# Kernel tuning notes

Hardware: AMD Instinct MI355X
Metric: run time of the kernel (lower is better)

The kernel has to match this reference:

```python
import jax, jax.numpy as jnp
import numpy as np

DIM = 1      # homological dimension
CARD = 50    # number of diagram points
H, W = 28, 28
D = 2        # len(Ip.shape)


def _cubical(X, dim=DIM, card=CARD):
    """Pure-numpy cubical persistence (gudhi semantics: lower-dim cells get the
    min of incident top-dimensional cells; finite pairs of dimension `dim`,
    positive persistence, sorted by persistence descending; returns flat
    (i,j) pixel indices of birth/death critical top cells, zero-padded to
    2*D*card int32 values). Mirrors the Cubical numpy_function in the repo."""
    X = np.asarray(X, dtype=np.float64)
    Hh, Ww = X.shape
    A, Bc = 2 * Hh - 1, 2 * Ww - 1
    n = A * Bc
    F = np.empty(n)                 # filtration value per cell
    P = np.empty(n, np.int64)       # flat pixel index of the top cell realizing F
    dms = np.empty(n, np.int64)     # cell dimension

    def cands(a, lim):
        if a % 2 == 1:
            return [(a - 1) // 2]
        return [r for r in (a // 2 - 1, a // 2) if 0 <= r < lim]

    for a in range(A):
        ris = cands(a, Hh)
        for b in range(Bc):
            cjs = cands(b, Ww)
            best = None
            bp = 0
            for r in ris:
                for c in cjs:
                    v = X[r, c]
                    if best is None or v < best:
                        best = v
                        bp = r * Ww + c
            idx = a * Bc + b
            F[idx] = best
            P[idx] = bp
            dms[idx] = (a & 1) + (b & 1)

    order = np.lexsort((np.arange(n), dms, F))   # sort by (F, dim, index)
    pos = np.empty(n, np.int64)
    pos[order] = np.arange(n)

    def faces(cell):
        a, b = divmod(cell, Bc)
        fs = []
        if a & 1:
            fs += [(a - 1) * Bc + b, (a + 1) * Bc + b]
        if b & 1:
            fs += [a * Bc + b - 1, a * Bc + b + 1]
        return fs

    # standard Z/2 boundary-matrix reduction
    Rcols = {}
    low_to_col = {}
    pairs = []
    for j in range(n):
        cell = order[j]
        col = set(int(pos[f]) for f in faces(cell))
        while col:
            l = max(col)
            k = low_to_col.get(l)
            if k is None:
                break
            col ^= Rcols[k]
        if col:
            l = max(col)
            low_to_col[l] = j
            Rcols[j] = col
            pairs.append((l, j))

    rows, pers = [], []
    for (i, j) in pairs:
        bc, dc = order[i], order[j]
        if dms[bc] != dim:
            continue
        pr = F[dc] - F[bc]
        if pr <= 0:
            continue
        rows.append((int(P[bc]), int(P[dc])))
        pers.append(pr)
    if rows:
        srt = np.argsort(np.asarray(pers))[::-1]   # persistence descending
        rows = [rows[k] for k in srt]

    inds = []
    for k in range(min(card, len(rows))):
        bi, di = rows[k]
        inds += [bi // Ww, bi % Ww, di // Ww, di % Ww]
    inds += [0] * (2 * D * card - len(inds))
    return np.asarray(inds, dtype=np.int32)


def setup_inputs() -> dict:
    key = jax.random.key(0)
    k1, k2 = jax.random.split(key)
    I = jax.random.normal(k1, (H, W, 2), dtype=jnp.float32)
    p = jax.random.normal(k2, (2, 1), dtype=jnp.float32)
    return {"I": I, "p": p}


def reference(I, p):
    # Ip = reshape(tensordot(I, p, 1), [28, 28])
    Ip = jnp.reshape(jnp.tensordot(I, p, 1), (H, W))
    inds = jax.pure_callback(
        lambda x: _cubical(np.asarray(x)),
        jax.ShapeDtypeStruct((2 * D * CARD,), jnp.int32),
        Ip,
    )
    inds = jax.lax.stop_gradient(inds).reshape(-1, D)   # [2*card, 2]
    # gather_nd(Ip, inds) then reshape to [card, 2]
    dgm = Ip[inds[:, 0], inds[:, 1]].reshape(-1, 2)
    return dgm
```

## Files before the change

kernel.cpp:

```cpp
#include <hip/hip_runtime.h>

#define IMG_H 28
#define IMG_W 28
#define AA 55
#define NCELL 3025
#define NEDGE 1512
#define NSQ 729
#define CARD 50
#define NW 24
#define CAP 160
#define BS 1024

typedef unsigned long long u64;
typedef unsigned int u32;
typedef unsigned short u16;

#define OFF_KEYSE   0
#define OFF_KEYSS   16384
#define OFF_IP      24576
#define OFF_RANKE   27712
#define OFF_RANKSQ  30736
#define OFF_COL     0
#define OFF_OWNB    30720
#define OFF_CANDA   0
#define OFF_CANDB   8192
#define OFF_BND     43008
#define OFF_EDGEF   48840
#define OFF_SQF     54888
#define OFF_CURLOW  58448
#define OFF_PAIRLOW 60832
#define OFF_NONAPP  62296
#define OFF_SCAL    63768
#define SMEM_TOTAL  63784

__device__ __forceinline__ int edgeCid(int a, int b) {
    return (a & 1) ? (((a - 1) >> 1) * 28 + (b >> 1))
                   : (756 + (a >> 1) * 27 + ((b - 1) >> 1));
}

__device__ __forceinline__ u32 sortable(float f) {
    u32 fb = __float_as_uint(f);
    return (fb & 0x80000000u) ? ~fb : (fb | 0x80000000u);
}
__device__ __forceinline__ float unsortable(u32 v) {
    return __uint_as_float((v & 0x80000000u) ? (v & 0x7FFFFFFFu) : ~v);
}

__device__ __forceinline__ u64 ldrelax(u64* p) {
    return __hip_atomic_load(p, __ATOMIC_RELAXED, __HIP_MEMORY_SCOPE_WORKGROUP);
}
__device__ __forceinline__ void strelax(u64* p, u64 v) {
    __hip_atomic_store(p, v, __ATOMIC_RELAXED, __HIP_MEMORY_SCOPE_WORKGROUP);
}

__device__ __forceinline__ u64 shflx64(u64 v, int s) {
    u32 lo = __shfl_xor((u32)v, s, 64);
    u32 hi = __shfl_xor((u32)(v >> 32), s, 64);
    return ((u64)hi << 32) | lo;
}

__device__ __forceinline__ void cswapDir(u64& a, u64& b, bool up) {
    u64 mn = a < b ? a : b, mx = a < b ? b : a;
    a = up ? mn : mx; b = up ? mx : mn;
}

__device__ __forceinline__ u64 bstage(u64 v, int i, int s, int size) {
    u64 p = shflx64(v, s);
    bool keepmin = (((i & size) == 0) == ((i & s) == 0));
    return keepmin ? (v < p ? v : p) : (v > p ? v : p);
}

__device__ __forceinline__ void sessA(u64& r0, u64& r1, int i0) {
    for (int size = 2; size <= 64; size <<= 1)
        for (int s = size >> 1; s; s >>= 1) {
            r0 = bstage(r0, i0, s, size);
            r1 = bstage(r1, i0 + 64, s, size);
        }
}
__device__ __forceinline__ void sessB(u64& r0, u64& r1, int i0, int size) {
    bool asc = ((i0 & size) == 0);
    { u64 mn = r0 < r1 ? r0 : r1, mx = r0 < r1 ? r1 : r0;
      r0 = asc ? mn : mx; r1 = asc ? mx : mn; }
    for (int s = 32; s; s >>= 1) {
        bool keep = (asc == ((i0 & s) == 0));
        u64 p0 = shflx64(r0, s);
        r0 = keep ? (r0 < p0 ? r0 : p0) : (r0 > p0 ? r0 : p0);
        u64 p1 = shflx64(r1, s);
        r1 = keep ? (r1 < p1 ? r1 : p1) : (r1 > p1 ? r1 : p1);
    }
}

template<int G>
__device__ __forceinline__ void fusedClassicArr(u64* arr, int nElem) {
    const int nG = nElem / G;
    for (int gid = (int)threadIdx.x; gid < nG; gid += BS) {
        int high = gid >> 7, low = gid & 127;
        bool up = ((high & 1) == 0);
        int base = high * G * 128 + low;
        u64 k[G];
        #pragma unroll
        for (int g = 0; g < G; ++g) k[g] = arr[base + g * 128];
        #pragma unroll
        for (int d = G / 2; d >= 1; d >>= 1)
            #pragma unroll
            for (int g = 0; g < G; ++g)
                if (!(g & d)) cswapDir(k[g], k[g | d], up);
        #pragma unroll
        for (int g = 0; g < G; ++g) arr[base + g * 128] = k[g];
    }
}

__device__ __forceinline__ void sessWin(u64* kE, u64* kS, int i0, int size, bool hasS) {
    u64 a = kE[i0], b = kE[i0 + 64];
    sessB(a, b, i0, size);
    kE[i0] = a; kE[i0 + 64] = b;
    if (hasS) {
        u64 c = kS[i0], d = kS[i0 + 64];
        sessB(c, d, i0, size);
        kS[i0] = c; kS[i0 + 64] = d;
    }
}

__device__ __forceinline__ u64 lstage(u64 v, int lane, int s, bool up) {
    u64 p = shflx64(v, s);
    bool keepmin = (up == ((lane & s) == 0));
    return keepmin ? (v < p ? v : p) : (v > p ? v : p);
}

__device__ __forceinline__ u64 sort64(u64 v, int lane) {
    for (int size = 2; size <= 32; size <<= 1)
        for (int s = size >> 1; s; s >>= 1)
            v = lstage(v, lane, s, (lane & size) == 0);
    for (int s = 32; s; s >>= 1)
        v = lstage(v, lane, s, true);
    return v;
}
__device__ __forceinline__ u64 merge64(u64 a, u64 b, int lane) {
    u64 br = shflx64(b, 63);
    u64 m = a < br ? a : br;
    for (int s = 32; s; s >>= 1)
        m = lstage(m, lane, s, true);
    return m;
}

__device__ __forceinline__ void xorInline(u64 o, u64& w, int lane) {
    #pragma unroll
    for (int q = 0; q < 4; ++q) {
        int rr = (int)((o >> (12 * q)) & 0xFFFull);
        if ((rr >> 6) == lane) w ^= 1ull << (rr & 63);
    }
}

__device__ __forceinline__ int findLow(u64 w, int lane) {
    u64 mask = __ballot(w != 0ull);
    if (mask == 0ull) return 0xFFFE;
    int L = 63 - __builtin_clzll(mask);
    int cand = (lane << 6) + 63 - __builtin_clzll(w | 1ull);
    return __builtin_amdgcn_readlane(cand, L);
}

__device__ __forceinline__ u64 bcast64lane0(u64 v) {
    u32 lo = __builtin_amdgcn_readfirstlane((u32)v);
    u32 hi = __builtin_amdgcn_readfirstlane((u32)(v >> 32));
    return ((u64)hi << 32) | lo;
}

__global__ __launch_bounds__(BS) void cubical_kernel(const float* __restrict__ I,
                                                     const float* __restrict__ p,
                                                     float* __restrict__ out) {
    __shared__ __align__(16) char smem[SMEM_TOTAL];
    u64*    keysE   = (u64*)(smem + OFF_KEYSE);
    u64*    keysS   = (u64*)(smem + OFF_KEYSS);
    float*  Ip      = (float*)(smem + OFF_IP);
    u16*    rankE   = (u16*)(smem + OFF_RANKE);
    u16*    rankSq  = (u16*)(smem + OFF_RANKSQ);
    u64*    col     = (u64*)(smem + OFF_COL);
    u64*    ownerBnd= (u64*)(smem + OFF_OWNB);
    u64*    candA   = (u64*)(smem + OFF_CANDA);
    u64*    candB   = (u64*)(smem + OFF_CANDB);
    u64*    bnd     = (u64*)(smem + OFF_BND);
    float*  edgeFr  = (float*)(smem + OFF_EDGEF);
    float*  sqF     = (float*)(smem + OFF_SQF);
    u16*    curLow  = (u16*)(smem + OFF_CURLOW);
    u16*    pairLow = (u16*)(smem + OFF_PAIRLOW);
    u16*    nonapp  = (u16*)(smem + OFF_NONAPP);
    float*  padvP   = (float*)(smem + OFF_SCAL);
    int*    Mp      = (int*)(smem + OFF_SCAL + 4);
    int*    tickP   = (int*)(smem + OFF_SCAL + 8);

    const int tid = threadIdx.x;
    const int wave = tid >> 6, lane = tid & 63;

    const float p0 = p[0], p1 = p[1];
    for (int i = tid; i < IMG_H * IMG_W; i += BS) {
        float v = I[2 * i] * p0 + I[2 * i + 1] * p1;
        Ip[i] = v;
        if (i == 0) *padvP = v;
    }
    for (int i = 1512 + tid; i < 2048; i += BS) keysE[i] = ~0ull;
    for (int i = 729 + tid; i < 1024; i += BS) keysS[i] = ~0ull;
    __syncthreads();

    for (int idx = tid; idx < NCELL; idx += BS) {
        int a = idx / AA, b = idx % AA;
        int da = a & 1, db = b & 1;
        int dim = da + db;
        if (dim == 0) continue;
        int r0, r1, c0, c1;
        if (da) { r0 = r1 = (a - 1) >> 1; }
        else    { r1 = a >> 1; r0 = (a == 0) ? r1 : r1 - 1; }
        if (db) { c0 = c1 = (b - 1) >> 1; }
        else    { c1 = b >> 1; c0 = (b == 0) ? c1 : c1 - 1; }
        float best = Ip[r0 * IMG_W + c0];
        best = fminf(best, Ip[r0 * IMG_W + c1]);
        best = fminf(best, Ip[r1 * IMG_W + c0]);
        best = fminf(best, Ip[r1 * IMG_W + c1]);
        u64 key = ((u64)sortable(best) << 12) | (u32)idx;
        if (dim == 1) keysE[edgeCid(a, b)] = key;
        else          keysS[((a - 1) >> 1) * 27 + ((b - 1) >> 1)] = key;
    }
    __syncthreads();

    {
        const int eB = wave * 128 + lane;
        const bool hasS = (wave < 8);
        {
            u64 a = keysE[eB], b = keysE[eB + 64];
            sessA(a, b, eB);
            sessB(a, b, eB, 128);
            keysE[eB] = a; keysE[eB + 64] = b;
            if (hasS) {
                u64 c = keysS[eB], d = keysS[eB + 64];
                sessA(c, d, eB);
                sessB(c, d, eB, 128);
                keysS[eB] = c; keysS[eB + 64] = d;
            }
        }
        __syncthreads();
        fusedClassicArr<2>(keysE, 2048);
        fusedClassicArr<2>(keysS, 1024);
        __syncthreads();
        sessWin(keysE, keysS, eB, 256, hasS);
        __syncthreads();
        fusedClassicArr<4>(keysE, 2048);
        fusedClassicArr<4>(keysS, 1024);
        __syncthreads();
        sessWin(keysE, keysS, eB, 512, hasS);
        __syncthreads();
        fusedClassicArr<8>(keysE, 2048);
        fusedClassicArr<8>(keysS, 1024);
        __syncthreads();
        sessWin(keysE, keysS, eB, 1024, hasS);
        __syncthreads();
        fusedClassicArr<16>(keysE, 2048);
        __syncthreads();
        sessWin(keysE, keysS, eB, 2048, false);
        __syncthreads();
    }

    for (int r = tid; r < NEDGE; r += BS) {
        u64 k = keysE[r];
        int idx = (int)(k & 0xFFFull);
        int a = idx / AA, b = idx % AA;
        rankE[edgeCid(a, b)] = (u16)r;
        edgeFr[r] = unsortable((u32)(k >> 12));
    }
    for (int r = tid; r < NSQ; r += BS) {
        u64 k = keysS[r];
        int idx = (int)(k & 0xFFFull);
        int a = idx / AA, b = idx % AA;
        rankSq[((a - 1) >> 1) * 27 + ((b - 1) >> 1)] = (u16)r;
        sqF[r] = unsortable((u32)(k >> 12));
    }
    __syncthreads();

    for (int j = tid; j < NSQ; j += BS) {
        int sidx = (int)(keysS[j] & 0xFFFull);
        int a = sidx / AA, b = sidx % AA;
        int ec[4] = { sidx - AA, sidx + AA, sidx - 1, sidx + 1 };
        int er[4];
        er[0] = rankE[edgeCid(a - 1, b)];
        er[1] = rankE[edgeCid(a + 1, b)];
        er[2] = rankE[edgeCid(a, b - 1)];
        er[3] = rankE[edgeCid(a, b + 1)];
        bnd[j] = (u64)er[0] | ((u64)er[1] << 16) | ((u64)er[2] << 32) | ((u64)er[3] << 48);
        int bq = 0;
        if (er[1] > er[bq]) bq = 1;
        if (er[2] > er[bq]) bq = 2;
        if (er[3] > er[bq]) bq = 3;
        int ecell = ec[bq];
        int x = ecell / AA, y = ecell % AA;
        u32 rmin = 0xFFFFFFFFu;
        if (x & 1) {
            if (y >= 2)  rmin = rankSq[((x - 1) >> 1) * 27 + ((y - 2) >> 1)];
            if (y <= 52) { u32 r2 = rankSq[((x - 1) >> 1) * 27 + (y >> 1)]; rmin = min(rmin, r2); }
        } else {
            if (x >= 2)  rmin = rankSq[((x - 2) >> 1) * 27 + ((y - 1) >> 1)];
            if (x <= 52) { u32 r2 = rankSq[(x >> 1) * 27 + ((y - 1) >> 1)]; rmin = min(rmin, r2); }
        }
        pairLow[j] = (rmin == (u32)j) ? (u16)(0x8000u | er[bq]) : (u16)0xFFFFu;
    }
    __syncthreads();

    for (int i = tid; i < 1536; i += BS) ownerBnd[i] = ~0ull;
    __syncthreads();
    for (int j = tid; j < NSQ; j += BS) {
        u16 pl = pairLow[j];
        if (pl != 0xFFFFu) {
            u64 bd = bnd[j];
            u64 e = (bd & 0xFFFull) | (((bd >> 16) & 0xFFFull) << 12)
                  | (((bd >> 32) & 0xFFFull) << 24) | (((bd >> 48) & 0xFFFull) << 36);
            ownerBnd[pl & 0x7FFF] = e;
        }
    }
    if (tid < 64) {
        int cnt = 0;
        for (int base = 0; base < NSQ; base += 64) {
            int j = base + lane;
            bool f = (j < NSQ) && (pairLow[j] == 0xFFFFu);
            u64 m = __ballot(f);
            int pfx = __popcll(m & ((1ull << lane) - 1ull));
            if (f) nonapp[cnt + pfx] = (u16)j;
            cnt += __popcll(m);
        }
        if (lane == 0) *Mp = (cnt > CAP) ? CAP : cnt;
    }
    __syncthreads();
    const int M = *Mp;

    for (int idx = tid; idx < M * NW; idx += BS) {
        int slot = idx / NW, w = idx - slot * NW;
        u64 bd = bnd[nonapp[slot]];
        u64 x = 0ull;
        #pragma unroll
        for (int q = 0; q < 4; ++q) {
            int rr = (int)((bd >> (16 * q)) & 0xFFFFull);
            if ((rr >> 6) == w) x ^= 1ull << (rr & 63);
        }
        col[idx] = x;
    }
    if (tid < M) {
        u64 bd = bnd[nonapp[tid]];
        int mx = 0;
        #pragma unroll
        for (int q = 0; q < 4; ++q) {
            int rr = (int)((bd >> (16 * q)) & 0xFFFFull);
            if (rr > mx) mx = rr;
        }
        curLow[tid] = (u16)mx;
    }
    if (tid == 0) *tickP = 16;
    __syncthreads();

    {
        int  slot = wave;
        bool act  = (slot < M);
        u64  enc  = (1ull << 63) | (u64)slot;
        u64  w    = 0ull;
        int  low  = 0;
        if (act) {
            if (lane < NW) w = ldrelax(&col[slot * NW + lane]);
            low = (int)curLow[slot];
        }
        while (act) {
            u64 o = ldrelax(&ownerBnd[low]);
            if (o < enc) {
                if (o >> 63) {
                    int s = (int)(o & 0xFFFull);
                    if (lane < NW) w ^= ldrelax(&col[s * NW + lane]);
                } else {
                    xorInline(o, w, lane);
                }
                low = findLow(w, lane);
                if (low != 0xFFFE) continue;
                if (lane == 0) curLow[slot] = (u16)0xFFFE;
            } else {
                if (lane < NW) strelax(&col[slot * NW + lane], w);
                __threadfence_block();
                u64 old = 0;
                if (lane == 0)
                    old = (u64)atomicMin((unsigned long long*)&ownerBnd[low],
                                         (unsigned long long)enc);
                old = bcast64lane0(old);
                if (old < enc) {
                    if (old >> 63) {
                        int s = (int)(old & 0xFFFull);
                        if (lane < NW) w ^= ldrelax(&col[s * NW + lane]);
                    } else {
                        xorInline(old, w, lane);
                    }
                    low = findLow(w, lane);
                    if (low != 0xFFFE) continue;
                    if (lane == 0) curLow[slot] = (u16)0xFFFE;
                } else {
                    if (lane == 0) curLow[slot] = (u16)low;
                    if (old != ~0ull) {
                        int vs = (int)(old & 0xFFFFull);
                        u64 cv = (lane < NW) ? ldrelax(&col[vs * NW + lane]) : 0ull;
                        w = cv ^ w;
                        slot = vs; enc = old;
                        low = findLow(w, lane);
                        if (low != 0xFFFE) continue;
                        if (lane == 0) curLow[slot] = (u16)0xFFFE;
                    }
                }
            }
            {
                u32 t = 0;
                if (lane == 0) t = (u32)atomicAdd(tickP, 1);
                t = (u32)__builtin_amdgcn_readfirstlane((int)t);
                if ((int)t < M) {
                    slot = (int)t;
                    enc  = (1ull << 63) | (u64)t;
                    w    = (lane < NW) ? ldrelax(&col[(int)t * NW + lane]) : 0ull;
                    low  = (int)curLow[t];
                } else {
                    act = false;
                }
            }
        }
        __syncthreads();
    }
    if (tid < M) {
        u16 cl = curLow[tid];
        pairLow[nonapp[tid]] = (cl == 0xFFFEu) ? (u16)0xFFFDu : cl;
    }
    __syncthreads();

    {
        if (wave < 12) {
            int i = wave * 64 + lane;
            u64 key = ~0ull;
            if (i < NSQ) {
                int pl = (int)pairLow[i];
                if (pl != 0xFFFD && pl != 0xFFFF) {
                    int low = pl & 0x7FFF;
                    double pr = (double)sqF[i] - (double)edgeFr[low];
                    if (pr > 0.0) {
                        u64 bits = (u64)__double_as_longlong(pr);
                        key = ~((bits & ~0xFFFull) | (u64)(u32)i);
                    }
                }
            }
            candA[wave * 64 + lane] = sort64(key, lane);
        }
        __syncthreads();
        if (wave < 6) {
            u64 a = candA[(2 * wave) * 64 + lane];
            u64 b = candA[(2 * wave + 1) * 64 + lane];
            candB[wave * 64 + lane] = merge64(a, b, lane);
        }
        __syncthreads();
        if (wave < 3) {
            u64 a = candB[(2 * wave) * 64 + lane];
            u64 b = candB[(2 * wave + 1) * 64 + lane];
            candA[wave * 64 + lane] = merge64(a, b, lane);
        }
        __syncthreads();
        if (wave == 0) {
            u64 a = candA[lane], b = candA[64 + lane], c = candA[128 + lane];
            u64 f = merge64(merge64(a, b, lane), c, lane);
            if (lane < CARD) {
                float bv, dv;
                if (f != ~0ull) {
                    u64 kb = ~f;
                    int j = (int)(kb & 0xFFFull);
                    int low = (int)pairLow[j] & 0x7FFF;
                    bv = edgeFr[low];
                    dv = sqF[j];
                } else {
                    bv = *padvP; dv = *padvP;
                }
                out[2 * lane]     = bv;
                out[2 * lane + 1] = dv;
            }
        }
    }
}

extern "C" void kernel_launch(void* const* d_in, const int* in_sizes, int n_in,
                              void* d_out, int out_size, void* d_ws, size_t ws_size,
                              hipStream_t stream) {
    const float* I = (const float*)d_in[0];
    const float* p = (const float*)d_in[1];
    float* out = (float*)d_out;
    hipLaunchKernelGGL(cubical_kernel, dim3(1), dim3(BS), 0, stream, I, p, out);
}
```

Measured before the change: 93.39 us.

## Batch-reduce all lanes' pivot hits per step in the wave-parallel column reduction

In the column reduction loop, each lane now looks up the owner of its own highest set bit in parallel. When the global low is already owned, the loop XORs in every qualifying lower-owned pivot found across lanes in one pass instead of one pivot per iteration, and findLow plus the precomputed initial curLow are removed. The aim is fewer serial iterations of the reduction loop and fewer owner lookups. The cost is more readlane and XOR work per iteration, and it changes the order in which columns are added, which could affect correctness if non-low pivot additions interact badly with concurrent ownership changes. It also widens the slot-index mask from 12 to 16 bits.

Result: slower. 98.47 us (+5.4%).

```diff
diff --git a/kernel.cpp b/kernel.cpp
--- a/kernel.cpp
+++ b/kernel.cpp
@@ -151,17 +151,25 @@
     }
 }
 
-__device__ __forceinline__ int findLow(u64 w, int lane) {
-    u64 mask = __ballot(w != 0ull);
-    if (mask == 0ull) return 0xFFFE;
-    int L = 63 - __builtin_clzll(mask);
-    int cand = (lane << 6) + 63 - __builtin_clzll(w | 1ull);
-    return __builtin_amdgcn_readlane(cand, L);
+__device__ __forceinline__ u64 appXorMask(u64 o, int lane) {
+    u64 x = 0ull;
+    #pragma unroll
+    for (int q = 0; q < 4; ++q) {
+        int rr = (int)((o >> (12 * q)) & 0xFFFull);
+        x ^= ((rr >> 6) == lane) ? (1ull << (rr & 63)) : 0ull;
+    }
+    return x;
 }
 
 __device__ __forceinline__ u64 bcast64lane0(u64 v) {
     u32 lo = __builtin_amdgcn_readfirstlane((u32)v);
     u32 hi = __builtin_amdgcn_readfirstlane((u32)(v >> 32));
+    return ((u64)hi << 32) | lo;
+}
+
+__device__ __forceinline__ u64 readlane64(u64 v, int l) {
+    u32 lo = (u32)__builtin_amdgcn_readlane((int)(u32)v, l);
+    u32 hi = (u32)__builtin_amdgcn_readlane((int)(u32)(v >> 32), l);
     return ((u64)hi << 32) | lo;
 }
 
@@ -339,16 +347,7 @@
         }
         col[idx] = x;
     }
-    if (tid < M) {
-        u64 bd = bnd[nonapp[tid]];
-        int mx = 0;
-        #pragma unroll
-        for (int q = 0; q < 4; ++q) {
-            int rr = (int)((bd >> (16 * q)) & 0xFFFFull);
-            if (rr > mx) mx = rr;
-        }
-        curLow[tid] = (u16)mx;
-    }
+    if (tid < M) curLow[tid] = (u16)0xFFFE;
     if (tid == 0) *tickP = 16;
     __syncthreads();
 
@@ -357,55 +356,67 @@
         bool act  = (slot < M);
         u64  enc  = (1ull << 63) | (u64)slot;
         u64  w    = 0ull;
-        int  low  = 0;
-        if (act) {
-            if (lane < NW) w = ldrelax(&col[slot * NW + lane]);
-            low = (int)curLow[slot];
-        }
+        if (act && lane < NW) w = ldrelax(&col[slot * NW + lane]);
+
         while (act) {
-            u64 o = ldrelax(&ownerBnd[low]);
-            if (o < enc) {
-                if (o >> 63) {
-                    int s = (int)(o & 0xFFFull);
-                    if (lane < NW) w ^= ldrelax(&col[s * NW + lane]);
-                } else {
-                    xorInline(o, w, lane);
-                }
-                low = findLow(w, lane);
-                if (low != 0xFFFE) continue;
+            bool has = (w != 0ull);
+            int  tl  = 63 - __builtin_clzll(w | 1ull);
+            int  pos = (lane << 6) + tl;
+            u64  o   = ldrelax(&ownerBnd[has ? pos : 0]);
+            u64  hm  = __ballot(has);
+            bool needRefill = false;
+            if (hm == 0ull) {
                 if (lane == 0) curLow[slot] = (u16)0xFFFE;
+                needRefill = true;
             } else {
+                int Ls = 63 - __builtin_clzll(hm);
+                u64 oG = readlane64(o, Ls);
+                if (oG < enc) {
+                    bool qual = has && (o < enc);
+                    u64 qm = __ballot(qual);
+                    u64 xacc = 0ull;
+                    while (qm) {
+                        int b = 63 - __builtin_clzll(qm);
+                        qm &= ~(1ull << b);
+                        u64 ob = readlane64(o, b);
+                        if (!(ob >> 63)) {
+                            xacc ^= appXorMask(ob, lane);
+                        } else {
+                            int s = (int)(ob & 0xFFFFull);
+                            if (lane < NW) xacc ^= ldrelax(&col[s * NW + lane]);
+                        }
+                    }
+                    w ^= xacc;
+                    continue;
+                }
+                int lowG = __builtin_amdgcn_readlane(pos, Ls);
                 if (lane < NW) strelax(&col[slot * NW + lane], w);
                 __threadfence_block();
                 u64 old = 0;
                 if (lane == 0)
-                    old = (u64)atomicMin((unsigned long long*)&ownerBnd[low],
+                    old = (u64)atomicMin((unsigned long long*)&ownerBnd[lowG],
                                          (unsigned long long)enc);
                 old = bcast64lane0(old);
                 if (old < enc) {
                     if (old >> 63) {
-                        int s = (int)(old & 0xFFFull);
+                        int s = (int)(old & 0xFFFFull);
                         if (lane < NW) w ^= ldrelax(&col[s * NW + lane]);
                     } else {
                         xorInline(old, w, lane);
                     }
-                    low = findLow(w, lane);
-                    if (low != 0xFFFE) continue;
-                    if (lane == 0) curLow[slot] = (u16)0xFFFE;
-                } else {
-                    if (lane == 0) curLow[slot] = (u16)low;
-                    if (old != ~0ull) {
-                        int vs = (int)(old & 0xFFFFull);
-                        u64 cv = (lane < NW) ? ldrelax(&col[vs * NW + lane]) : 0ull;
-                        w = cv ^ w;
-                        slot = vs; enc = old;
-                        low = findLow(w, lane);
-                        if (low != 0xFFFE) continue;
-                        if (lane == 0) curLow[slot] = (u16)0xFFFE;
-                    }
-                }
+                    continue;
+                }
+                if (lane == 0) curLow[slot] = (u16)lowG;
+                if (old != ~0ull) {
+                    int vs = (int)(old & 0xFFFFull);
+                    u64 cv = (lane < NW) ? ldrelax(&col[vs * NW + lane]) : 0ull;
+                    w = cv ^ w;
+                    slot = vs; enc = old;
+                    continue;
+                }
+                needRefill = true;
             }
-            {
+            if (needRefill) {
                 u32 t = 0;
                 if (lane == 0) t = (u32)atomicAdd(tickP, 1);
                 t = (u32)__builtin_amdgcn_readfirstlane((int)t);
@@ -413,7 +424,6 @@
                     slot = (int)t;
                     enc  = (1ull << 63) | (u64)t;
                     w    = (lane < NW) ? ldrelax(&col[(int)t * NW + lane]) : 0ull;
-                    low  = (int)curLow[t];
                 } else {
                     act = false;
                 }
```
